# Performance work log

Hardware: AMD Instinct MI355X
Metric: run time of the kernel (lower is better)

The kernel has to match this reference:

```python
import jax, jax.numpy as jnp
import numpy as np
import math

W = 64  # window_size == chunk_size == 64


def _windows(x, w):
    """x: [b, t, ...] -> [b, nb, 2w, ...]: for block j, concat(block j-1, block j).
    Block -1 is zero padding; its validity is handled by the attention mask."""
    b, t = x.shape[0], x.shape[1]
    nb = t // w
    pad = [(0, 0), (w, 0)] + [(0, 0)] * (x.ndim - 2)
    xp = jnp.pad(x, pad)                                   # [b, t+w, ...]
    xb = xp.reshape((b, nb + 1, w) + x.shape[2:])          # [b, nb+1, w, ...]
    return jnp.concatenate([xb[:, :-1], xb[:, 1:]], axis=2)  # [b, nb, 2w, ...]


def setup_inputs() -> dict:
    key = jax.random.key(0)
    k1, k2, k3 = jax.random.split(key, 3)
    b, t, h, d = 4, 4096, 16, 64
    return {
        "q": jax.random.normal(k1, (b, t, h, d), dtype=jnp.float32),
        "k": jax.random.normal(k2, (b, t, h, d), dtype=jnp.float32),
        "v": jax.random.normal(k3, (b, t, h, d), dtype=jnp.float32),
        "attn_mask": jnp.ones((b, t), dtype=jnp.int32),
    }


def reference(q, k, v, attn_mask):
    b, t, h, d = q.shape
    nb = t // W
    scale = 1.0 / math.sqrt(d)

    qb = q.reshape(b, nb, W, h, d)
    kw = _windows(k, W)                         # [b, nb, 2W, h, d]
    vw = _windows(v, W)                         # [b, nb, 2W, h, d]
    mw = _windows(attn_mask.astype(bool), W)    # [b, nb, 2W]

    # query local index i attends to key local index m iff 0 <= (i+W-m) < W
    i = jnp.arange(W)[:, None]
    m = jnp.arange(2 * W)[None, :]
    diff = i + W - m
    band = (diff >= 0) & (diff < W)             # [W, 2W]

    valid = band[None, None] & mw[:, :, None, :]          # [b, nb, W, 2W]

    scores = jnp.einsum('bnqhd,bnkhd->bnhqk', qb, kw) * scale  # [b,nb,h,W,2W]
    scores = jnp.where(valid[:, :, None], scores, jnp.float32(-1e9))
    attn = jax.nn.softmax(scores, axis=-1)
    attn = attn * valid[:, :, None].astype(attn.dtype)

    qm = attn_mask.astype(q.dtype).reshape(b, nb, W)      # query validity
    attn = attn * qm[:, :, None, :, None]

    out = jnp.einsum('bnhqk,bnkhd->bnqhd', attn, vw)      # [b,nb,W,h,d]
    out = out * qm[:, :, :, None, None]
    return out.reshape(b, t, h, d)
```

## Files before the change

kernel.cpp:

```cpp
#include <hip/hip_runtime.h>


#define TT 4096
#define HH 16
#define DD 64
#define WW 64
#define NBLK (TT / WW)

typedef __attribute__((ext_vector_type(8))) short bf16x8;
typedef __attribute__((ext_vector_type(16))) float f32x16;

static __device__ __forceinline__ uint bfr(float x) {
    uint u = __builtin_bit_cast(uint, x);
    return (u + 0x7FFFu + ((u >> 16) & 1u)) >> 16;
}
static __device__ __forceinline__ ushort f2bf(float x) { return (ushort)bfr(x); }
static __device__ __forceinline__ uint pack2(float a, float b) {
    return bfr(a) | (bfr(b) << 16);
}
static __device__ __forceinline__ int vsw(int d) { return ((d >> 2) ^ d) & 15; }

__global__ __launch_bounds__(128, 6)
void lca_fwd(const float* __restrict__ q, const float* __restrict__ k,
             const float* __restrict__ v, const int* __restrict__ am,
             float* __restrict__ out)
{
    const int jb = ((blockIdx.x & 7) << 3) | (blockIdx.x >> 3);
    const int hd = blockIdx.y;
    const int bi = blockIdx.z;

    __shared__ __align__(16) ushort sVt[8192];

    const int tid  = threadIdx.x;
    const int wv   = tid >> 6;
    const int lane = tid & 63;
    const int l31  = lane & 31, hl = lane >> 5;

    const int T0 = jb * WW;
    const int Tq = T0 + 32 * wv;
    const size_t rowstride = (size_t)HH * DD;
    const size_t hoff = ((size_t)bi * TT) * rowstride + (size_t)hd * DD;
    const int* amb = am + (size_t)bi * TT;

    long tok0 = (long)Tq - 64 + lane;
    int am_lo = amb[tok0 < 0 ? 0 : tok0];
    int am_hi = amb[Tq + l31];

    float4 vq[8], vk[24], vv[16];
    {
        const float* qr = q + hoff + (size_t)(Tq + l31) * rowstride + hl * 8;
        #pragma unroll
        for (int ds = 0; ds < 4; ++ds) {
            vq[2 * ds]     = *(const float4*)(qr + ds * 16);
            vq[2 * ds + 1] = *(const float4*)(qr + ds * 16 + 4);
        }
    }
    #pragma unroll
    for (int t = 0; t < 3; ++t) {
        long krw = (long)Tq - 64 + 32 * t + l31;
        const float* kr = k + hoff + (size_t)(krw < 0 ? 0 : krw) * rowstride + hl * 8;
        #pragma unroll
        for (int ds = 0; ds < 4; ++ds) {
            vk[8 * t + 2 * ds]     = *(const float4*)(kr + ds * 16);
            vk[8 * t + 2 * ds + 1] = *(const float4*)(kr + ds * 16 + 4);
        }
    }
    const int d0 = (tid & 15) * 4;
    const int rb = tid >> 4;
    #pragma unroll
    for (int p = 0; p < 16; ++p) {
        int kl = p * 8 + rb;
        long tok = (long)T0 - 64 + kl;
        if (tok < 0) tok = 0;
        vv[p] = *(const float4*)(v + hoff + (size_t)tok * rowstride + d0);
    }

    unsigned long long m_lo = __ballot((tok0 >= 0) && (am_lo != 0));
    unsigned int m_hi = (unsigned int)__ballot(am_hi != 0);
    const bool fastmask = (m_lo == ~0ull) && (m_hi == 0xFFFFFFFFu);

    bf16x8 Bq[4];
    #pragma unroll
    for (int ds = 0; ds < 4; ++ds) {
        union { bf16x8 v8; uint u[4]; } w;
        w.u[0] = pack2(vq[2 * ds].x,     vq[2 * ds].y);
        w.u[1] = pack2(vq[2 * ds].z,     vq[2 * ds].w);
        w.u[2] = pack2(vq[2 * ds + 1].x, vq[2 * ds + 1].y);
        w.u[3] = pack2(vq[2 * ds + 1].z, vq[2 * ds + 1].w);
        Bq[ds] = w.v8;
    }

    float s[48];
    #pragma unroll
    for (int t = 0; t < 3; ++t) {
        f32x16 a;
        #pragma unroll
        for (int i = 0; i < 16; ++i) a[i] = 0.f;
        #pragma unroll
        for (int ds = 0; ds < 4; ++ds) {
            union { bf16x8 v8; uint u[4]; } w;
            w.u[0] = pack2(vk[8 * t + 2 * ds].x,     vk[8 * t + 2 * ds].y);
            w.u[1] = pack2(vk[8 * t + 2 * ds].z,     vk[8 * t + 2 * ds].w);
            w.u[2] = pack2(vk[8 * t + 2 * ds + 1].x, vk[8 * t + 2 * ds + 1].y);
            w.u[3] = pack2(vk[8 * t + 2 * ds + 1].z, vk[8 * t + 2 * ds + 1].w);
            a = __builtin_amdgcn_mfma_f32_32x32x16_bf16(w.v8, Bq[ds], a, 0, 0, 0);
        }
        #pragma unroll
        for (int r = 0; r < 16; ++r) s[t * 16 + r] = a[r];
    }

    const int ql = l31;
    float mx[24];
    #pragma unroll
    for (int i = 0; i < 24; ++i) mx[i] = fmaxf(s[i], s[i + 24]);
    #pragma unroll
    for (int i = 0; i < 12; ++i) mx[i] = fmaxf(mx[i], mx[i + 12]);
    #pragma unroll
    for (int i = 0; i < 6;  ++i) mx[i] = fmaxf(mx[i], mx[i + 6]);
    float rmax = fmaxf(fmaxf(fmaxf(mx[0], mx[1]), fmaxf(mx[2], mx[3])),
                       fmaxf(mx[4], mx[5]));
    rmax = fmaxf(rmax, __shfl_xor(rmax, 32, 64));

    const float CEXP = 0.125f * 1.44269504088896f;
    float p[48];
    #pragma unroll
    for (int t = 0; t < 3; ++t)
        #pragma unroll
        for (int r = 0; r < 16; ++r) {
            int i  = t * 16 + r;
            int kl = 32 * t + (r & 3) + 8 * (r >> 2) + 4 * hl;
            float pe = exp2f((s[i] - rmax) * CEXP);
            bool band = (t == 0) ? (kl > ql) : (t == 2 ? (kl - 64 <= ql) : true);
            pe = band ? pe : 0.f;
            if (!fastmask) {
                uint bit = (kl < 64) ? (uint)((m_lo >> kl) & 1ull)
                                     : ((m_hi >> (kl - 64)) & 1u);
                pe *= (float)bit;
            }
            p[i] = pe;
        }

    float t24[24];
    #pragma unroll
    for (int i = 0; i < 24; ++i) t24[i] = p[i] + p[i + 24];
    #pragma unroll
    for (int i = 0; i < 12; ++i) t24[i] += t24[i + 12];
    #pragma unroll
    for (int i = 0; i < 6;  ++i) t24[i] += t24[i + 6];
    float sum = ((t24[0] + t24[1]) + (t24[2] + t24[3])) + (t24[4] + t24[5]);
    sum += __shfl_xor(sum, 32, 64);

    float rden = (sum > 0.f ? 1.f / sum : 0.f) * (float)((m_hi >> ql) & 1u);

    uint pk[24];
    #pragma unroll
    for (int m = 0; m < 24; ++m)
        pk[m] = pack2(p[2 * m] * rden, p[2 * m + 1] * rden);

    #pragma unroll
    for (int pp = 0; pp < 16; ++pp) {
        int kl = pp * 8 + rb;
        const float4 x = vv[pp];
        int e = kl & 15;
        int pos = (kl & ~15) | (e & 3) | ((e & 8) >> 1) | ((e & 4) << 1);
        int pu = pos >> 3, p7 = pos & 7;
        sVt[(d0 + 0) * 128 + ((pu ^ vsw(d0 + 0)) << 3) + p7] = f2bf(x.x);
        sVt[(d0 + 1) * 128 + ((pu ^ vsw(d0 + 1)) << 3) + p7] = f2bf(x.y);
        sVt[(d0 + 2) * 128 + ((pu ^ vsw(d0 + 2)) << 3) + p7] = f2bf(x.z);
        sVt[(d0 + 3) * 128 + ((pu ^ vsw(d0 + 3)) << 3) + p7] = f2bf(x.w);
    }

    __syncthreads();

    f32x16 O0, O1;
    #pragma unroll
    for (int i = 0; i < 16; ++i) { O0[i] = 0.f; O1[i] = 0.f; }
    #pragma unroll
    for (int st = 0; st < 6; ++st) {
        union { bf16x8 v8; uint u[4]; } A;
        const int mb = 8 * (st >> 1) + 4 * (st & 1);
        #pragma unroll
        for (int j = 0; j < 4; ++j) A.u[j] = pk[mb + j];
        const int Ub = 4 * wv + 2 * st + hl;
        {
            int d = l31;
            const bf16x8 B0 = *(const bf16x8*)(&sVt[d * 128 + ((Ub ^ vsw(d)) << 3)]);
            O0 = __builtin_amdgcn_mfma_f32_32x32x16_bf16(A.v8, B0, O0, 0, 0, 0);
        }
        {
            int d = 32 + l31;
            const bf16x8 B1 = *(const bf16x8*)(&sVt[d * 128 + ((Ub ^ vsw(d)) << 3)]);
            O1 = __builtin_amdgcn_mfma_f32_32x32x16_bf16(A.v8, B1, O1, 0, 0, 0);
        }
    }

    float* ob = out + hoff + (size_t)Tq * rowstride;
    #pragma unroll
    for (int r = 0; r < 16; ++r) {
        int qrow = (r & 3) + 8 * (r >> 2) + 4 * hl;
        float* orow = ob + (size_t)qrow * rowstride;
        orow[l31]      = O0[r];
        orow[32 + l31] = O1[r];
    }
}

extern "C" void kernel_launch(void* const* d_in, const int* in_sizes, int n_in,
                              void* d_out, int out_size, void* d_ws, size_t ws_size,
                              hipStream_t stream) {
    const float* q  = (const float*)d_in[0];
    const float* k  = (const float*)d_in[1];
    const float* v  = (const float*)d_in[2];
    const int*   am = (const int*)d_in[3];
    float* outp = (float*)d_out;

    const int b = in_sizes[3] / TT;
    dim3 grid(NBLK, HH, b);
    dim3 block(128);
    lca_fwd<<<grid, block, 0, stream>>>(q, k, v, am, outp);
}
```

Baseline: 232.3 us.

## Load V directly from global per wave, dropping LDS transpose and barrier

Removes the shared-memory staging of V, where the block loaded all 128 V rows, converted them to bf16 and transposed them into LDS before a __syncthreads. Each wave now gathers its own MFMA B operands with scalar global loads and packs them to bf16 in registers. This frees LDS and removes the barrier, but the per-lane 4-byte strided loads are less coalesced than the old float4 loads, overlapping key windows are re-read from global/L2 by both waves, and the V loads no longer overlap the QK/softmax phase. The occupancy hint in launch bounds is lowered from 6 to 5.

```diff
diff --git a/kernel.cpp b/kernel.cpp
--- a/kernel.cpp
+++ b/kernel.cpp
@@ -14,13 +14,11 @@
     uint u = __builtin_bit_cast(uint, x);
     return (u + 0x7FFFu + ((u >> 16) & 1u)) >> 16;
 }
-static __device__ __forceinline__ ushort f2bf(float x) { return (ushort)bfr(x); }
 static __device__ __forceinline__ uint pack2(float a, float b) {
     return bfr(a) | (bfr(b) << 16);
 }
-static __device__ __forceinline__ int vsw(int d) { return ((d >> 2) ^ d) & 15; }
-
-__global__ __launch_bounds__(128, 6)
+
+__global__ __launch_bounds__(128, 5)
 void lca_fwd(const float* __restrict__ q, const float* __restrict__ k,
              const float* __restrict__ v, const int* __restrict__ am,
              float* __restrict__ out)
@@ -29,8 +27,6 @@
     const int hd = blockIdx.y;
     const int bi = blockIdx.z;
 
-    __shared__ __align__(16) ushort sVt[8192];
-
     const int tid  = threadIdx.x;
     const int wv   = tid >> 6;
     const int lane = tid & 63;
@@ -46,7 +42,7 @@
     int am_lo = amb[tok0 < 0 ? 0 : tok0];
     int am_hi = amb[Tq + l31];
 
-    float4 vq[8], vk[24], vv[16];
+    float4 vq[8], vk[24];
     {
         const float* qr = q + hoff + (size_t)(Tq + l31) * rowstride + hl * 8;
         #pragma unroll
@@ -64,15 +60,6 @@
             vk[8 * t + 2 * ds]     = *(const float4*)(kr + ds * 16);
             vk[8 * t + 2 * ds + 1] = *(const float4*)(kr + ds * 16 + 4);
         }
-    }
-    const int d0 = (tid & 15) * 4;
-    const int rb = tid >> 4;
-    #pragma unroll
-    for (int p = 0; p < 16; ++p) {
-        int kl = p * 8 + rb;
-        long tok = (long)T0 - 64 + kl;
-        if (tok < 0) tok = 0;
-        vv[p] = *(const float4*)(v + hoff + (size_t)tok * rowstride + d0);
     }
 
     unsigned long long m_lo = __ballot((tok0 >= 0) && (am_lo != 0));
@@ -157,41 +144,34 @@
     for (int m = 0; m < 24; ++m)
         pk[m] = pack2(p[2 * m] * rden, p[2 * m + 1] * rden);
 
-    #pragma unroll
-    for (int pp = 0; pp < 16; ++pp) {
-        int kl = pp * 8 + rb;
-        const float4 x = vv[pp];
-        int e = kl & 15;
-        int pos = (kl & ~15) | (e & 3) | ((e & 8) >> 1) | ((e & 4) << 1);
-        int pu = pos >> 3, p7 = pos & 7;
-        sVt[(d0 + 0) * 128 + ((pu ^ vsw(d0 + 0)) << 3) + p7] = f2bf(x.x);
-        sVt[(d0 + 1) * 128 + ((pu ^ vsw(d0 + 1)) << 3) + p7] = f2bf(x.y);
-        sVt[(d0 + 2) * 128 + ((pu ^ vsw(d0 + 2)) << 3) + p7] = f2bf(x.z);
-        sVt[(d0 + 3) * 128 + ((pu ^ vsw(d0 + 3)) << 3) + p7] = f2bf(x.w);
-    }
-
-    __syncthreads();
-
     f32x16 O0, O1;
     #pragma unroll
     for (int i = 0; i < 16; ++i) { O0[i] = 0.f; O1[i] = 0.f; }
+    const float* vbase = v + hoff;
     #pragma unroll
     for (int st = 0; st < 6; ++st) {
         union { bf16x8 v8; uint u[4]; } A;
         const int mb = 8 * (st >> 1) + 4 * (st & 1);
         #pragma unroll
         for (int j = 0; j < 4; ++j) A.u[j] = pk[mb + j];
-        const int Ub = 4 * wv + 2 * st + hl;
-        {
-            int d = l31;
-            const bf16x8 B0 = *(const bf16x8*)(&sVt[d * 128 + ((Ub ^ vsw(d)) << 3)]);
-            O0 = __builtin_amdgcn_mfma_f32_32x32x16_bf16(A.v8, B0, O0, 0, 0, 0);
-        }
-        {
-            int d = 32 + l31;
-            const bf16x8 B1 = *(const bf16x8*)(&sVt[d * 128 + ((Ub ^ vsw(d)) << 3)]);
-            O1 = __builtin_amdgcn_mfma_f32_32x32x16_bf16(A.v8, B1, O1, 0, 0, 0);
-        }
+
+        float b0f[8], b1f[8];
+        #pragma unroll
+        for (int j = 0; j < 8; ++j) {
+            long tr = (long)Tq - 64 + 16 * st + 4 * hl + (j & 3) + 8 * (j >> 2);
+            if (tr < 0) tr = 0;
+            const float* vr = vbase + (size_t)tr * rowstride;
+            b0f[j] = vr[l31];
+            b1f[j] = vr[32 + l31];
+        }
+        union { bf16x8 v8; uint u[4]; } B0, B1;
+        #pragma unroll
+        for (int j = 0; j < 4; ++j) {
+            B0.u[j] = pack2(b0f[2 * j], b0f[2 * j + 1]);
+            B1.u[j] = pack2(b1f[2 * j], b1f[2 * j + 1]);
+        }
+        O0 = __builtin_amdgcn_mfma_f32_32x32x16_bf16(A.v8, B0.v8, O0, 0, 0, 0);
+        O1 = __builtin_amdgcn_mfma_f32_32x32x16_bf16(A.v8, B1.v8, O1, 0, 0, 0);
     }
 
     float* ob = out + hoff + (size_t)Tq * rowstride;
```

Result: slower. 246.5 us (+6.1%).
